# Kernel optimization log

Measured on AMD Instinct MI355X. Metric: run time of the kernel, lower is better.

The kernel has to match this reference:

```python
import jax, jax.numpy as jnp
import numpy as np

EPS = 1e-5

def conv2d(x, w, b, stride, pad):
    out = jax.lax.conv_general_dilated(x, w, (stride, stride), [(pad, pad), (pad, pad)], dimension_numbers=('NCHW', 'OIHW', 'NCHW'))
    return out + b[None, :, None, None]

def instance_norm(x):
    m = jnp.mean(x, axis=(2, 3), keepdims=True)
    v = jnp.mean((x - m) ** 2, axis=(2, 3), keepdims=True)
    return (x - m) * jax.lax.rsqrt(v + EPS)

def mod_deform_conv(x, w, b, ow, ob, stride, pad):
    # Modulated deformable conv v2 (groups=1, deformable_groups=1, dilation=1).
    B, Cin, H, W = x.shape
    Cout, _, K, _ = w.shape
    P = K * K
    om = conv2d(x, ow, ob, stride, pad)            # [B, 3P, Ho, Wo] offset/mask predictor
    o1, o2, m = jnp.split(om, 3, axis=1)
    offset = jnp.concatenate([o1, o2], axis=1)     # [B, 2P, Ho, Wo]
    mask = jax.nn.sigmoid(m)                       # [B, P, Ho, Wo]
    Ho, Wo = om.shape[2], om.shape[3]
    off = offset.reshape(B, P, 2, Ho, Wo)          # interleaved (dy, dx) per kernel point
    dy, dx = off[:, :, 0], off[:, :, 1]
    ky, kx = jnp.meshgrid(jnp.arange(K), jnp.arange(K), indexing='ij')
    base_y = (jnp.arange(Ho) * stride - pad)[None, :, None] + ky.reshape(P)[:, None, None]
    base_x = (jnp.arange(Wo) * stride - pad)[None, None, :] + kx.reshape(P)[:, None, None]
    py = base_y[None].astype(x.dtype) + dy         # [B, P, Ho, Wo]
    px = base_x[None].astype(x.dtype) + dx
    y0 = jnp.floor(py); x0 = jnp.floor(px)
    wy = py - y0; wx = px - x0
    def gather(xb, yi, xi):
        return xb[:, yi, xi]                       # [Cin, P, Ho, Wo]
    acc = jnp.zeros((B, Cin, P, Ho, Wo), x.dtype)
    for oy, ox_, wgt in ((0.0, 0.0, (1 - wy) * (1 - wx)), (0.0, 1.0, (1 - wy) * wx), (1.0, 0.0, wy * (1 - wx)), (1.0, 1.0, wy * wx)):
        yy = y0 + oy; xx = x0 + ox_
        valid = (yy >= 0) & (yy <= H - 1) & (xx >= 0) & (xx <= W - 1)
        yc = jnp.clip(yy, 0, H - 1).astype(jnp.int32)
        xc = jnp.clip(xx, 0, W - 1).astype(jnp.int32)
        v = jax.vmap(gather)(x, yc, xc)            # [B, Cin, P, Ho, Wo]
        acc = acc + v * (wgt * valid)[:, None]
    cols = acc * mask[:, None]
    out = jnp.einsum('bcphw,ocp->bohw', cols, w.reshape(Cout, Cin, P))
    return out + b[None, :, None, None]

def _forward(x, d1w, d1b, d1ow, d1ob, d2w, d2b, d2ow, d2ob, d3w, d3b, d3ow, d3ob, d4w, d4b, d4ow, d4ob, res_w, res_b):
    h = jax.nn.relu(instance_norm(mod_deform_conv(x, d1w, d1b, d1ow, d1ob, 1, 3)))
    h = jax.nn.relu(instance_norm(mod_deform_conv(h, d2w, d2b, d2ow, d2ob, 2, 1)))
    h = jax.nn.relu(instance_norm(mod_deform_conv(h, d3w, d3b, d3ow, d3ob, 2, 1)))
    h = jax.nn.relu(instance_norm(mod_deform_conv(h, d4w, d4b, d4ow, d4ob, 2, 1)))
    for i in range(res_w.shape[0]):
        r = jax.nn.relu(instance_norm(conv2d(h, res_w[i, 0], res_b[i, 0], 1, 1)))
        r = instance_norm(conv2d(r, res_w[i, 1], res_b[i, 1], 1, 1))
        h = h + 0.1 * r
    return h

def setup_inputs():
    key = jax.random.key(0)
    ks = jax.random.split(key, 24)
    B, H, W = 8, 256, 256
    NF, MC = 3, 64
    def w_init(k, shape):
        fan_in = float(np.prod(shape[1:]))
        return jax.random.normal(k, shape, jnp.float32) / np.sqrt(fan_in)
    inp = {'x': jax.random.normal(ks[0], (B, NF, H, W), jnp.float32)}
    chans = [(NF, MC // 2, 7), (MC // 2, MC, 4), (MC, 2 * MC, 4), (2 * MC, 4 * MC, 4)]
    i = 1
    for n, (ci, co, k) in enumerate(chans, 1):
        inp[f'dcn{n}_w'] = w_init(ks[i], (co, ci, k, k)); i += 1
        inp[f'dcn{n}_b'] = 0.01 * jax.random.normal(ks[i], (co,), jnp.float32); i += 1
        P3 = 3 * k * k
        inp[f'dcn{n}_ow'] = 0.01 * jax.random.normal(ks[i], (P3, ci, k, k), jnp.float32); i += 1
        inp[f'dcn{n}_ob'] = 0.01 * jax.random.normal(ks[i], (P3,), jnp.float32); i += 1
    C, NR = 4 * MC, 2
    inp['res_w'] = w_init(ks[i], (NR, 2, C, C, 3, 3)); i += 1
    inp['res_b'] = 0.01 * jax.random.normal(ks[i], (NR, 2, C), jnp.float32)
    return inp

def reference(x, dcn1_w, dcn1_b, dcn1_ow, dcn1_ob, dcn2_w, dcn2_b, dcn2_ow, dcn2_ob, dcn3_w, dcn3_b, dcn3_ow, dcn3_ob, dcn4_w, dcn4_b, dcn4_ow, dcn4_ob, res_w, res_b):
    return _forward(x, dcn1_w, dcn1_b, dcn1_ow, dcn1_ob, dcn2_w, dcn2_b, dcn2_ow, dcn2_ob, dcn3_w, dcn3_b, dcn3_ow, dcn3_ob, dcn4_w, dcn4_b, dcn4_ow, dcn4_ob, res_w, res_b)
```

## Files before the change

kernel.cpp:

```cpp
#include <hip/hip_runtime.h>
#include <hip/hip_bf16.h>
#include <math.h>

#define EPS 1e-5f

typedef short bfrag8 __attribute__((ext_vector_type(8)));
typedef float f32x4 __attribute__((ext_vector_type(4)));
typedef unsigned short ushort_t;

__device__ inline ushort_t f2bf(float f) {
    __hip_bfloat16 h = __float2bfloat16(f);
    return *reinterpret_cast<ushort_t*>(&h);
}
__device__ inline float bf2f(ushort_t u) {
    unsigned int v = ((unsigned int)u) << 16;
    float f;
    __builtin_memcpy(&f, &v, 4);
    return f;
}

__global__ __launch_bounds__(256) void pack_w_kernel(
    const float* __restrict__ src, ushort_t* __restrict__ dst,
    int M, int R, int Mpad, int Rpad)
{
    const int idx = blockIdx.x * 256 + threadIdx.x;
    if (idx >= Mpad * Rpad) return;
    const int m = idx / Rpad, r = idx % Rpad;
    float v = 0.0f;
    if (m < M && r < R) v = src[(size_t)m * R + r];
    dst[idx] = f2bf(v);
}

template<int CIN, int COUT, int K, int STRIDE, int PAD, int TILE, int PMODE>
__global__ __launch_bounds__(256, 4) void dcn_mfma_kernel(
    const float* __restrict__ x, int H, int W,
    const ushort_t* __restrict__ wpk,
    const float* __restrict__ bias,
    const ushort_t* __restrict__ owpk,
    const float* __restrict__ ob,
    float* __restrict__ out, int Ho, int Wo)
{
    constexpr int P     = K * K;
    constexpr int P3    = 3 * P;
    constexpr int R     = CIN * P;
    constexpr int Rpad  = (R + 63) & ~63;
    constexpr int KT    = Rpad / 32;
    constexpr int NT    = (TILE + 15) / 16;
    constexpr int MT1   = (P3 + 15) / 16;
    constexpr int MT1PW = (MT1 + 3) / 4;
    constexpr int MT3   = COUT / 16;
    constexpr int MT3PW = (MT3 + 3) / 4;
    constexpr int COLS  = (TILE - 1) * STRIDE + K;
    constexpr int PROWS = K + 2;
    constexpr int PCOLS = COLS + 2;
    constexpr int PELN  = CIN * PROWS * PCOLS;
    constexpr int P32   = (PMODE == 2) ? PELN : (PMODE == 3) ? (PELN + 1) / 2 : 1;
    constexpr int LRLIM = (TILE < 16) ? TILE : 16;

    __shared__ unsigned int s_patch32[P32];
    __shared__ ushort_t s_u[TILE * Rpad];
    __shared__ float s_py[TILE][P];
    __shared__ float s_px[TILE][P];
    __shared__ ushort_t s_mask[TILE][P];

    ushort_t* s_patchh = (ushort_t*)s_patch32;
    float*    s_patchf = (float*)s_patch32;

    const int tilesPerImg = (Ho * Wo) / TILE;
    const int b    = blockIdx.x / tilesPerImg;
    const int tile = blockIdx.x % tilesPerImg;
    const int base = tile * TILE;
    const int tid  = threadIdx.x;
    const int wid  = tid >> 6, lane = tid & 63;
    const int lr   = lane & 15;
    const int lk8  = (lane >> 4) * 8;

    const int oy0 = base / Wo;
    const int ox0 = base % Wo;
    const int iy0 = oy0 * STRIDE - PAD;
    const int ix0 = ox0 * STRIDE - PAD;

    const float* xb = x + (size_t)b * CIN * H * W;

    if constexpr (PMODE == 2 || PMODE == 3) {
        for (int idx = tid; idx < PELN; idx += 256) {
            const int c   = idx / (PROWS * PCOLS);
            const int rem = idx % (PROWS * PCOLS);
            const int pr  = rem / PCOLS;
            const int pc_ = rem % PCOLS;
            const int iy = iy0 - 1 + pr, ix = ix0 - 1 + pc_;
            float v = 0.0f;
            if (iy >= 0 && iy < H && ix >= 0 && ix < W)
                v = xb[(size_t)c * H * W + iy * W + ix];
            if constexpr (PMODE == 2) s_patchf[idx] = v;
            else                      s_patchh[idx] = f2bf(v);
        }
        __syncthreads();
    }

    for (int rr = tid; rr < Rpad; rr += 256) {
        if (rr < R) {
            const int c = rr / P, p = rr % P;
            const int ky = p / K, kx = p % K;
            if constexpr (PMODE == 2) {
                const float* srcrow =
                    &s_patchf[(c * PROWS + ky + 1) * PCOLS + kx + 1];
                #pragma unroll 4
                for (int pix = 0; pix < TILE; ++pix)
                    s_u[pix * Rpad + (rr ^ ((pix & 7) << 3))] =
                        f2bf(srcrow[pix * STRIDE]);
            } else if constexpr (PMODE == 3) {
                const ushort_t* srcrow =
                    &s_patchh[(c * PROWS + ky + 1) * PCOLS + kx + 1];
                #pragma unroll 4
                for (int pix = 0; pix < TILE; ++pix)
                    s_u[pix * Rpad + (rr ^ ((pix & 7) << 3))] =
                        srcrow[pix * STRIDE];
            } else {
                const int iy = iy0 + ky;
                const bool rowok = (iy >= 0 && iy < H);
                const float* xrow = xb + (size_t)c * H * W +
                                    (size_t)(rowok ? iy : 0) * W;
                #pragma unroll 4
                for (int pix = 0; pix < TILE; ++pix) {
                    const int ix = ix0 + pix * STRIDE + kx;
                    float v = 0.0f;
                    if (rowok && ix >= 0 && ix < W) v = xrow[ix];
                    s_u[pix * Rpad + (rr ^ ((pix & 7) << 3))] = f2bf(v);
                }
            }
        } else {
            #pragma unroll 4
            for (int pix = 0; pix < TILE; ++pix)
                s_u[pix * Rpad + (rr ^ ((pix & 7) << 3))] = 0;
        }
    }
    __syncthreads();

    {
        f32x4 acc1[MT1PW][NT] = {};
        for (int kt = 0; kt < KT; ++kt) {
            bfrag8 bfr[NT];
            #pragma unroll
            for (int nt = 0; nt < NT; ++nt)
                bfr[nt] = *(const bfrag8*)&s_u[(nt * 16 + lr) * Rpad +
                              ((kt * 32 + lk8) ^ ((lr & 7) << 3))];
            #pragma unroll
            for (int i = 0; i < MT1PW; ++i) {
                const int mt = wid + 4 * i;
                if (mt < MT1) {
                    const bfrag8 afr = *(const bfrag8*)&owpk[
                        (size_t)(mt * 16 + lr) * Rpad + kt * 32 + lk8];
                    #pragma unroll
                    for (int nt = 0; nt < NT; ++nt)
                        acc1[i][nt] = __builtin_amdgcn_mfma_f32_16x16x32_bf16(
                            afr, bfr[nt], acc1[i][nt], 0, 0, 0);
                }
            }
        }
        if (lr < LRLIM) {
            #pragma unroll
            for (int i = 0; i < MT1PW; ++i) {
                const int mt = wid + 4 * i;
                if (mt < MT1) {
                    #pragma unroll
                    for (int nt = 0; nt < NT; ++nt) {
                        const int pix = nt * 16 + lr;
                        #pragma unroll
                        for (int q = 0; q < 4; ++q) {
                            const int ch = mt * 16 + (lane >> 4) * 4 + q;
                            if (ch < P3) {
                                const float v = acc1[i][nt][q] + ob[ch];
                                if (ch < 2 * P) {
                                    const int p = ch >> 1;
                                    if (ch & 1)
                                        s_px[pix][p] = (float)(ix0 + pix * STRIDE
                                                               + p % K) + v;
                                    else
                                        s_py[pix][p] = (float)(iy0 + p / K) + v;
                                } else {
                                    s_mask[pix][ch - 2 * P] =
                                        f2bf(1.0f / (1.0f + __expf(-v)));
                                }
                            }
                        }
                    }
                }
            }
        }
    }
    __syncthreads();

    {
        constexpr int ITEMS = TILE * P;
        constexpr int CG  = (ITEMS >= 256) ? 1 : (256 / ITEMS);
        constexpr int CPG = CIN / CG;
        constexpr int PSZ = PROWS * PCOLS;
        const int HW = H * W;
        for (int it = tid; it < ITEMS * CG; it += 256) {
            int item, cg;
            if constexpr (CG == 1) { item = it; cg = 0; }
            else { item = it % ITEMS; cg = it / ITEMS; }
            const int p   = item % P;
            const int pix = item / P;
            const float py = s_py[pix][p];
            const float px = s_px[pix][p];
            const float mk = bf2f(s_mask[pix][p]);
            const float y0f = floorf(py), x0f = floorf(px);
            const float wy = py - y0f, wx = px - x0f;
            const int y0 = (int)y0f, x0 = (int)x0f;
            const int swz = (pix & 7) << 3;
            ushort_t* dst = &s_u[pix * Rpad];
            bool done = false;
            if constexpr (PMODE == 2) {
                const int pyr = y0 - (iy0 - 1);
                const int pxr = x0 - (ix0 - 1);
                if (pyr >= 0 && pyr < PROWS - 1 && pxr >= 0 && pxr < PCOLS - 1) {
                    const float* pp = &s_patchf[(size_t)(cg * CPG) * PSZ
                                                + pyr * PCOLS + pxr];
                    int c = cg * CPG;
                    #pragma unroll
                    for (int ci = 0; ci < CPG; ++ci, ++c) {
                        const float v00 = pp[0], v01 = pp[1];
                        const float v10 = pp[PCOLS], v11 = pp[PCOLS + 1];
                        const float top = v00 + wx * (v01 - v00);
                        const float bot = v10 + wx * (v11 - v10);
                        const float acc = top + wy * (bot - top);
                        dst[(c * P + p) ^ swz] = f2bf(acc * mk);
                        pp += PSZ;
                    }
                    done = true;
                }
            } else if constexpr (PMODE == 3) {
                const int pyr = y0 - (iy0 - 1);
                const int pxr = x0 - (ix0 - 1);
                if (pyr >= 0 && pyr < PROWS - 1 && pxr >= 0 && pxr < PCOLS - 1) {
                    const ushort_t* pp = &s_patchh[(size_t)(cg * CPG) * PSZ
                                                   + pyr * PCOLS + pxr];
                    int c = cg * CPG;
                    #pragma unroll 4
                    for (int ci = 0; ci < CPG; ++ci, ++c) {
                        const float v00 = bf2f(pp[0]), v01 = bf2f(pp[1]);
                        const float v10 = bf2f(pp[PCOLS]), v11 = bf2f(pp[PCOLS + 1]);
                        const float top = v00 + wx * (v01 - v00);
                        const float bot = v10 + wx * (v11 - v10);
                        const float acc = top + wy * (bot - top);
                        dst[(c * P + p) ^ swz] = f2bf(acc * mk);
                        pp += PSZ;
                    }
                    done = true;
                }
            }
            if (!done) {
                if (y0 >= 0 && y0 < H - 1 && x0 >= 0 && x0 < W - 1) {
                    const float* pr = xb + (size_t)(cg * CPG) * HW
                                         + (size_t)y0 * W + x0;
                    int c = cg * CPG;
                    for (int ci = 0; ci < CPG; ++ci, ++c) {
                        const float v00 = pr[0], v01 = pr[1];
                        const float v10 = pr[W], v11 = pr[W + 1];
                        const float top = v00 + wx * (v01 - v00);
                        const float bot = v10 + wx * (v11 - v10);
                        const float acc = top + wy * (bot - top);
                        dst[(c * P + p) ^ swz] = f2bf(acc * mk);
                        pr += HW;
                    }
                } else {
                    const bool y0ok = (y0 >= 0 && y0 < H);
                    const bool y1ok = (y0 + 1 >= 0 && y0 + 1 < H);
                    const bool x0ok = (x0 >= 0 && x0 < W);
                    const bool x1ok = (x0 + 1 >= 0 && x0 + 1 < W);
                    const float w00 = (1.0f - wy) * (1.0f - wx);
                    const float w01 = (1.0f - wy) * wx;
                    const float w10 = wy * (1.0f - wx);
                    const float w11 = wy * wx;
                    const float* xc = xb + (size_t)(cg * CPG) * HW;
                    int c = cg * CPG;
                    for (int ci = 0; ci < CPG; ++ci, ++c) {
                        float acc = 0.0f;
                        if (y0ok) {
                            const float* pr = xc + (size_t)y0 * W + x0;
                            if (x0ok) acc += pr[0] * w00;
                            if (x1ok) acc += pr[1] * w01;
                        }
                        if (y1ok) {
                            const float* pr = xc + (size_t)(y0 + 1) * W + x0;
                            if (x0ok) acc += pr[0] * w10;
                            if (x1ok) acc += pr[1] * w11;
                        }
                        dst[(c * P + p) ^ swz] = f2bf(acc * mk);
                        xc += HW;
                    }
                }
            }
        }
        if constexpr (Rpad != R) {
            for (int idx = tid; idx < (Rpad - R) * TILE; idx += 256) {
                const int r   = R + idx / TILE;
                const int pix = idx % TILE;
                s_u[pix * Rpad + (r ^ ((pix & 7) << 3))] = 0;
            }
        }
    }
    __syncthreads();

    {
        f32x4 acc3[MT3PW][NT] = {};
        for (int kt = 0; kt < KT; ++kt) {
            bfrag8 bfr[NT];
            #pragma unroll
            for (int nt = 0; nt < NT; ++nt)
                bfr[nt] = *(const bfrag8*)&s_u[(nt * 16 + lr) * Rpad +
                              ((kt * 32 + lk8) ^ ((lr & 7) << 3))];
            #pragma unroll
            for (int i = 0; i < MT3PW; ++i) {
                const int mt = wid + 4 * i;
                if (mt < MT3) {
                    const bfrag8 afr = *(const bfrag8*)&wpk[
                        (size_t)(mt * 16 + lr) * Rpad + kt * 32 + lk8];
                    #pragma unroll
                    for (int nt = 0; nt < NT; ++nt)
                        acc3[i][nt] = __builtin_amdgcn_mfma_f32_16x16x32_bf16(
                            afr, bfr[nt], acc3[i][nt], 0, 0, 0);
                }
            }
        }
        if (lr < LRLIM) {
            #pragma unroll
            for (int i = 0; i < MT3PW; ++i) {
                const int mt = wid + 4 * i;
                if (mt < MT3) {
                    #pragma unroll
                    for (int nt = 0; nt < NT; ++nt) {
                        #pragma unroll
                        for (int q = 0; q < 4; ++q) {
                            const int ch = mt * 16 + (lane >> 4) * 4 + q;
                            out[(((size_t)b * COUT + ch) * Ho + oy0) * Wo
                                + ox0 + nt * 16 + lr] = acc3[i][nt][q] + bias[ch];
                        }
                    }
                }
            }
        }
    }
}

template<int BS>
__global__ __launch_bounds__(BS) void in_relu_kernel(float* __restrict__ data,
                                                     int HW, int relu)
{
    float* plane = data + (size_t)blockIdx.x * HW;
    const int tid = threadIdx.x;
    float s = 0.0f, s2 = 0.0f;
    for (int i = tid * 4; i < HW; i += BS * 4) {
        const float4 v = *(const float4*)&plane[i];
        s  += v.x + v.y + v.z + v.w;
        s2 += v.x * v.x + v.y * v.y + v.z * v.z + v.w * v.w;
    }
    __shared__ float red0[BS];
    __shared__ float red1[BS];
    red0[tid] = s; red1[tid] = s2;
    __syncthreads();
    for (int off = BS / 2; off > 0; off >>= 1) {
        if (tid < off) { red0[tid] += red0[tid + off]; red1[tid] += red1[tid + off]; }
        __syncthreads();
    }
    const float mean = red0[0] / (float)HW;
    float var = red1[0] / (float)HW - mean * mean;
    var = fmaxf(var, 0.0f);
    const float rstd = rsqrtf(var + EPS);
    for (int i = tid * 4; i < HW; i += BS * 4) {
        float4 v = *(const float4*)&plane[i];
        v.x = (v.x - mean) * rstd; v.y = (v.y - mean) * rstd;
        v.z = (v.z - mean) * rstd; v.w = (v.w - mean) * rstd;
        if (relu) {
            v.x = fmaxf(v.x, 0.0f); v.y = fmaxf(v.y, 0.0f);
            v.z = fmaxf(v.z, 0.0f); v.w = fmaxf(v.w, 0.0f);
        }
        *(float4*)&plane[i] = v;
    }
}

__global__ __launch_bounds__(256) void in_resadd_kernel(float* __restrict__ h,
                                                        const float* __restrict__ r,
                                                        int HW)
{
    const float* plane = r + (size_t)blockIdx.x * HW;
    float* hp = h + (size_t)blockIdx.x * HW;
    const int tid = threadIdx.x;
    float s = 0.0f, s2 = 0.0f;
    for (int i = tid * 4; i < HW; i += 1024) {
        const float4 v = *(const float4*)&plane[i];
        s  += v.x + v.y + v.z + v.w;
        s2 += v.x * v.x + v.y * v.y + v.z * v.z + v.w * v.w;
    }
    __shared__ float red0[256];
    __shared__ float red1[256];
    red0[tid] = s; red1[tid] = s2;
    __syncthreads();
    for (int off = 128; off > 0; off >>= 1) {
        if (tid < off) { red0[tid] += red0[tid + off]; red1[tid] += red1[tid + off]; }
        __syncthreads();
    }
    const float mean = red0[0] / (float)HW;
    float var = red1[0] / (float)HW - mean * mean;
    var = fmaxf(var, 0.0f);
    const float rstd = rsqrtf(var + EPS);
    for (int i = tid * 4; i < HW; i += 1024) {
        const float4 v = *(const float4*)&plane[i];
        float4 o = *(const float4*)&hp[i];
        o.x += 0.1f * ((v.x - mean) * rstd);
        o.y += 0.1f * ((v.y - mean) * rstd);
        o.z += 0.1f * ((v.z - mean) * rstd);
        o.w += 0.1f * ((v.w - mean) * rstd);
        *(float4*)&hp[i] = o;
    }
}

__global__ __launch_bounds__(256) void in_resadd_out_kernel(
    float* __restrict__ dst, const float* __restrict__ h,
    const float* __restrict__ r, int HW)
{
    const float* plane = r + (size_t)blockIdx.x * HW;
    const float* hp = h + (size_t)blockIdx.x * HW;
    float* dp = dst + (size_t)blockIdx.x * HW;
    const int tid = threadIdx.x;
    float s = 0.0f, s2 = 0.0f;
    for (int i = tid * 4; i < HW; i += 1024) {
        const float4 v = *(const float4*)&plane[i];
        s  += v.x + v.y + v.z + v.w;
        s2 += v.x * v.x + v.y * v.y + v.z * v.z + v.w * v.w;
    }
    __shared__ float red0[256];
    __shared__ float red1[256];
    red0[tid] = s; red1[tid] = s2;
    __syncthreads();
    for (int off = 128; off > 0; off >>= 1) {
        if (tid < off) { red0[tid] += red0[tid + off]; red1[tid] += red1[tid + off]; }
        __syncthreads();
    }
    const float mean = red0[0] / (float)HW;
    float var = red1[0] / (float)HW - mean * mean;
    var = fmaxf(var, 0.0f);
    const float rstd = rsqrtf(var + EPS);
    for (int i = tid * 4; i < HW; i += 1024) {
        const float4 v = *(const float4*)&plane[i];
        const float4 o = *(const float4*)&hp[i];
        float4 d;
        d.x = o.x + 0.1f * ((v.x - mean) * rstd);
        d.y = o.y + 0.1f * ((v.y - mean) * rstd);
        d.z = o.z + 0.1f * ((v.z - mean) * rstd);
        d.w = o.w + 0.1f * ((v.w - mean) * rstd);
        *(float4*)&dp[i] = d;
    }
}

__global__ __launch_bounds__(256) void im2col_tiled_kernel(
    const float* __restrict__ in, ushort_t* __restrict__ cols)
{
    const int bid = blockIdx.x;
    const int cg = bid & 3;
    const int y  = (bid >> 2) & 31;
    const int b  = bid >> 7;
    const int c0 = cg * 64;
    const int tid = threadIdx.x;

    __shared__ float s_p[64 * 3 * 34];

    for (int idx = tid; idx < 64 * 3 * 34; idx += 256) {
        const int c   = idx / 102;
        const int rem = idx % 102;
        const int r   = rem / 34;
        const int xx  = rem % 34;
        const int yy = y + r - 1;
        const int gx = xx - 1;
        float v = 0.0f;
        if (yy >= 0 && yy < 32 && gx >= 0 && gx < 32)
            v = in[(((size_t)b * 256 + c0 + c) * 32 + yy) * 32 + gx];
        s_p[idx] = v;
    }
    __syncthreads();

    for (int it = tid; it < 512; it += 256) {
        const int xout = it >> 4;
        const int cq   = (it & 15) * 4;
        const int n = b * 1024 + y * 32 + xout;
        ushort_t* oc = cols + (size_t)n * 2304 + (size_t)(c0 + cq) * 9;
        ushort_t tmp[36];
        #pragma unroll
        for (int ci = 0; ci < 4; ++ci)
            #pragma unroll
            for (int ky = 0; ky < 3; ++ky)
                #pragma unroll
                for (int kx = 0; kx < 3; ++kx)
                    tmp[ci * 9 + ky * 3 + kx] =
                        f2bf(s_p[(cq + ci) * 102 + ky * 34 + xout + kx]);
        #pragma unroll
        for (int i2 = 0; i2 < 9; ++i2) {
            unsigned long long w =
                  (unsigned long long)tmp[4 * i2]
                | ((unsigned long long)tmp[4 * i2 + 1] << 16)
                | ((unsigned long long)tmp[4 * i2 + 2] << 32)
                | ((unsigned long long)tmp[4 * i2 + 3] << 48);
            *((unsigned long long*)oc + i2) = w;
        }
    }
}

__global__ __launch_bounds__(256) void f32_to_bf16_kernel(
    const float* __restrict__ in, ushort_t* __restrict__ out, int n)
{
    const int i = blockIdx.x * 256 + threadIdx.x;
    if (i < n) out[i] = f2bf(in[i]);
}

__global__ __launch_bounds__(512) void gemm_bf16_kernel(
    const ushort_t* __restrict__ A,
    const ushort_t* __restrict__ Bt,
    const float* __restrict__ bias,
    float* __restrict__ C)
{
    constexpr int Kt = 2304;
    __shared__ ushort_t sA[64][72];
    __shared__ ushort_t sB[128][72];

    const int m0 = blockIdx.x * 64;
    const int n0 = blockIdx.y * 128;
    const int tid  = threadIdx.x;
    const int wid  = tid >> 6, lane = tid & 63;
    const int wm = wid & 1, wn = wid >> 1;
    const int lr = lane & 15, lk = (lane >> 4) * 8;

    const int srow = tid >> 3, sseg = (tid & 7) * 8;
    const ushort_t* ap  = A  + (size_t)(m0 + srow) * Kt + sseg;
    const ushort_t* bp0 = Bt + (size_t)(n0 + srow) * Kt + sseg;
    const ushort_t* bp1 = Bt + (size_t)(n0 + 64 + srow) * Kt + sseg;

    f32x4 acc[2][2] = {};

    for (int k0 = 0; k0 < Kt; k0 += 64) {
        __syncthreads();
        *(int4*)&sA[srow][sseg]      = *(const int4*)(ap + k0);
        *(int4*)&sB[srow][sseg]      = *(const int4*)(bp0 + k0);
        *(int4*)&sB[64 + srow][sseg] = *(const int4*)(bp1 + k0);
        __syncthreads();

        #pragma unroll
        for (int ks = 0; ks < 2; ++ks) {
            bfrag8 af[2], bf[2];
            #pragma unroll
            for (int mi = 0; mi < 2; ++mi)
                af[mi] = *(const bfrag8*)&sA[wm * 32 + mi * 16 + lr][ks * 32 + lk];
            #pragma unroll
            for (int nj = 0; nj < 2; ++nj)
                bf[nj] = *(const bfrag8*)&sB[wn * 32 + nj * 16 + lr][ks * 32 + lk];
            #pragma unroll
            for (int mi = 0; mi < 2; ++mi)
                #pragma unroll
                for (int nj = 0; nj < 2; ++nj)
                    acc[mi][nj] = __builtin_amdgcn_mfma_f32_16x16x32_bf16(
                        af[mi], bf[nj], acc[mi][nj], 0, 0, 0);
        }
    }

    #pragma unroll
    for (int mi = 0; mi < 2; ++mi) {
        #pragma unroll
        for (int nj = 0; nj < 2; ++nj) {
            const int n = n0 + wn * 32 + nj * 16 + lr;
            const int b = n >> 10, pix = n & 1023;
            #pragma unroll
            for (int r = 0; r < 4; ++r) {
                const int m = m0 + wm * 32 + mi * 16 + (lane >> 4) * 4 + r;
                C[(((size_t)b * 256 + m) << 10) + pix] = acc[mi][nj][r] + bias[m];
            }
        }
    }
}

extern "C" void kernel_launch(void* const* d_in, const int* in_sizes, int n_in,
                              void* d_out, int out_size, void* d_ws, size_t ws_size,
                              hipStream_t stream)
{
    const float* x    = (const float*)d_in[0];
    const float* d1w  = (const float*)d_in[1];
    const float* d1b  = (const float*)d_in[2];
    const float* d1ow = (const float*)d_in[3];
    const float* d1ob = (const float*)d_in[4];
    const float* d2w  = (const float*)d_in[5];
    const float* d2b  = (const float*)d_in[6];
    const float* d2ow = (const float*)d_in[7];
    const float* d2ob = (const float*)d_in[8];
    const float* d3w  = (const float*)d_in[9];
    const float* d3b  = (const float*)d_in[10];
    const float* d3ow = (const float*)d_in[11];
    const float* d3ob = (const float*)d_in[12];
    const float* d4w  = (const float*)d_in[13];
    const float* d4b  = (const float*)d_in[14];
    const float* d4ow = (const float*)d_in[15];
    const float* d4ob = (const float*)d_in[16];
    const float* resw = (const float*)d_in[17];
    const float* resb = (const float*)d_in[18];

    float* A   = (float*)d_ws;
    float* Bb  = A + 16777216;
    float* out = (float*)d_out;

    ushort_t* pk = (ushort_t*)d_out;
    ushort_t* ow1 = pk;
    ushort_t* w1  = ow1 + 160 * 192;
    ushort_t* ow2 = w1  + 32 * 192;
    ushort_t* w2  = ow2 + 48 * 512;
    ushort_t* ow3 = w2  + 64 * 512;
    ushort_t* w3  = ow3 + 48 * 1024;
    ushort_t* ow4 = w3  + 128 * 1024;
    ushort_t* w4  = ow4 + 48 * 2048;

    float* r    = A;
    float* r2   = A + 2097152;
    ushort_t* cols = (ushort_t*)(A + 4194304);
    ushort_t* wbf  = (ushort_t*)Bb;
    float* H4   = Bb + 4194304;

    const int B = 8;

    pack_w_kernel<<<(160 * 192 + 255) / 256, 256, 0, stream>>>(d1ow, ow1, 147, 147, 160, 192);
    pack_w_kernel<<<(32 * 192 + 255) / 256, 256, 0, stream>>>(d1w, w1, 32, 147, 32, 192);
    pack_w_kernel<<<(48 * 512 + 255) / 256, 256, 0, stream>>>(d2ow, ow2, 48, 512, 48, 512);
    pack_w_kernel<<<(64 * 512 + 255) / 256, 256, 0, stream>>>(d2w, w2, 64, 512, 64, 512);
    pack_w_kernel<<<(48 * 1024 + 255) / 256, 256, 0, stream>>>(d3ow, ow3, 48, 1024, 48, 1024);
    pack_w_kernel<<<(128 * 1024 + 255) / 256, 256, 0, stream>>>(d3w, w3, 128, 1024, 128, 1024);
    pack_w_kernel<<<(48 * 2048 + 255) / 256, 256, 0, stream>>>(d4ow, ow4, 48, 2048, 48, 2048);
    pack_w_kernel<<<(256 * 2048 + 255) / 256, 256, 0, stream>>>(d4w, w4, 256, 2048, 256, 2048);

    dcn_mfma_kernel<3, 32, 7, 1, 3, 32, 2><<<B * (256 * 256 / 32), 256, 0, stream>>>(
        x, 256, 256, w1, d1b, ow1, d1ob, A, 256, 256);
    in_relu_kernel<1024><<<B * 32, 1024, 0, stream>>>(A, 65536, 1);

    dcn_mfma_kernel<32, 64, 4, 2, 1, 16, 3><<<B * (128 * 128 / 16), 256, 0, stream>>>(
        A, 256, 256, w2, d2b, ow2, d2ob, Bb, 128, 128);
    in_relu_kernel<1024><<<B * 64, 1024, 0, stream>>>(Bb, 16384, 1);

    dcn_mfma_kernel<64, 128, 4, 2, 1, 8, 3><<<B * (64 * 64 / 8), 256, 0, stream>>>(
        Bb, 128, 128, w3, d3b, ow3, d3ob, A, 64, 64);
    in_relu_kernel<1024><<<B * 128, 1024, 0, stream>>>(A, 4096, 1);

    dcn_mfma_kernel<128, 256, 4, 2, 1, 8, 0><<<B * (32 * 32 / 8), 256, 0, stream>>>(
        A, 64, 64, w4, d4b, ow4, d4ob, H4, 32, 32);
    in_relu_kernel<256><<<B * 256, 256, 0, stream>>>(H4, 1024, 1);

    f32_to_bf16_kernel<<<(4 * 589824 + 255) / 256, 256, 0, stream>>>(
        resw, wbf, 4 * 589824);

    dim3 ggrid(4, 64);
    im2col_tiled_kernel<<<1024, 256, 0, stream>>>(H4, cols);
    gemm_bf16_kernel<<<ggrid, 512, 0, stream>>>(
        wbf + (size_t)0 * 589824, cols, resb + 0 * 256, r);
    in_relu_kernel<256><<<B * 256, 256, 0, stream>>>(r, 1024, 1);
    im2col_tiled_kernel<<<1024, 256, 0, stream>>>(r, cols);
    gemm_bf16_kernel<<<ggrid, 512, 0, stream>>>(
        wbf + (size_t)1 * 589824, cols, resb + 1 * 256, r2);
    in_resadd_kernel<<<B * 256, 256, 0, stream>>>(H4, r2, 1024);

    im2col_tiled_kernel<<<1024, 256, 0, stream>>>(H4, cols);
    gemm_bf16_kernel<<<ggrid, 512, 0, stream>>>(
        wbf + (size_t)2 * 589824, cols, resb + 2 * 256, r);
    in_relu_kernel<256><<<B * 256, 256, 0, stream>>>(r, 1024, 1);
    im2col_tiled_kernel<<<1024, 256, 0, stream>>>(r, cols);
    gemm_bf16_kernel<<<ggrid, 512, 0, stream>>>(
        wbf + (size_t)3 * 589824, cols, resb + 3 * 256, r2);
    in_resadd_out_kernel<<<B * 256, 256, 0, stream>>>(out, H4, r2, 1024);
}
```

Measured before the change: 1.230 ms.

## Double-buffer LDS tiles in bf16 GEMM with register prefetch

The residual-block GEMM kernel now keeps two LDS buffers and loads the next K-tile from global memory into registers while MFMAs run on the current tile. The registers are written to the alternate buffer afterwards, so each iteration needs one barrier instead of two. This aims to hide global load latency behind compute, at the cost of doubled shared memory and more live registers.

Result: no change. 1.218 ms (-1.0%).

```diff
diff --git a/kernel.cpp b/kernel.cpp
--- a/kernel.cpp
+++ b/kernel.cpp
@@ -521,8 +521,9 @@
     float* __restrict__ C)
 {
     constexpr int Kt = 2304;
-    __shared__ ushort_t sA[64][72];
-    __shared__ ushort_t sB[128][72];
+    constexpr int NTILES = Kt / 64;
+    __shared__ ushort_t sA[2][64][72];
+    __shared__ ushort_t sB[2][128][72];
 
     const int m0 = blockIdx.x * 64;
     const int n0 = blockIdx.y * 128;
@@ -538,22 +539,31 @@
 
     f32x4 acc[2][2] = {};
 
-    for (int k0 = 0; k0 < Kt; k0 += 64) {
-        __syncthreads();
-        *(int4*)&sA[srow][sseg]      = *(const int4*)(ap + k0);
-        *(int4*)&sB[srow][sseg]      = *(const int4*)(bp0 + k0);
-        *(int4*)&sB[64 + srow][sseg] = *(const int4*)(bp1 + k0);
-        __syncthreads();
-
+    int4 ra  = *(const int4*)(ap);
+    int4 rb0 = *(const int4*)(bp0);
+    int4 rb1 = *(const int4*)(bp1);
+    *(int4*)&sA[0][srow][sseg]      = ra;
+    *(int4*)&sB[0][srow][sseg]      = rb0;
+    *(int4*)&sB[0][64 + srow][sseg] = rb1;
+    __syncthreads();
+
+    for (int t = 0; t < NTILES; ++t) {
+        const int cur = t & 1;
+        if (t + 1 < NTILES) {
+            const int k0 = (t + 1) * 64;
+            ra  = *(const int4*)(ap + k0);
+            rb0 = *(const int4*)(bp0 + k0);
+            rb1 = *(const int4*)(bp1 + k0);
+        }
         #pragma unroll
         for (int ks = 0; ks < 2; ++ks) {
             bfrag8 af[2], bf[2];
             #pragma unroll
             for (int mi = 0; mi < 2; ++mi)
-                af[mi] = *(const bfrag8*)&sA[wm * 32 + mi * 16 + lr][ks * 32 + lk];
+                af[mi] = *(const bfrag8*)&sA[cur][wm * 32 + mi * 16 + lr][ks * 32 + lk];
             #pragma unroll
             for (int nj = 0; nj < 2; ++nj)
-                bf[nj] = *(const bfrag8*)&sB[wn * 32 + nj * 16 + lr][ks * 32 + lk];
+                bf[nj] = *(const bfrag8*)&sB[cur][wn * 32 + nj * 16 + lr][ks * 32 + lk];
             #pragma unroll
             for (int mi = 0; mi < 2; ++mi)
                 #pragma unroll
@@ -561,6 +571,12 @@
                     acc[mi][nj] = __builtin_amdgcn_mfma_f32_16x16x32_bf16(
                         af[mi], bf[nj], acc[mi][nj], 0, 0, 0);
         }
+        if (t + 1 < NTILES) {
+            *(int4*)&sA[cur ^ 1][srow][sseg]      = ra;
+            *(int4*)&sB[cur ^ 1][srow][sseg]      = rb0;
+            *(int4*)&sB[cur ^ 1][64 + srow][sseg] = rb1;
+        }
+        __syncthreads();
     }
 
     #pragma unroll
```
